# Kernel optimization log

Hardware: AMD Instinct MI355X
Metric: run time of the kernel (lower is better)

## Reference

```python
import jax, jax.numpy as jnp
import numpy as np

EPS = 1e-4

def _mlp2(x, W1, b1, W2, b2):
    # Sequential(Linear, ReLU, Linear) -> [*, 1]
    return jax.nn.relu(x @ W1 + b1) @ W2 + b2

def setup_inputs() -> dict:
    N, D = 400, 64
    key = jax.random.key(0)
    ks = jax.random.split(key, 24)
    s = 0.1
    inp = {
        "t": 0,
        "node_edge_embedding": jax.random.normal(ks[0], (N + N * N, D), jnp.float32),
        "node_flow_norm": jax.random.normal(ks[1], (N, D), jnp.float32),
        "A_ne": jax.random.uniform(ks[2], (N, N * N), jnp.float32),
        "node_num": N,
        # alpha_n_dedunce
        "W_alpha": jax.random.normal(ks[3], (D, D), jnp.float32) * s,
        "b_alpha": jnp.zeros((D,), jnp.float32),
        # gamma_e_dedunce
        "W_gamma": jax.random.normal(ks[4], (D, D), jnp.float32) * s,
        "b_gamma": jnp.zeros((D,), jnp.float32),
        # node_to_edge (2D -> D)
        "W_n2e": jax.random.normal(ks[5], (2 * D, D), jnp.float32) * s,
        "b_n2e": jnp.zeros((D,), jnp.float32),
        # edge_to_value: D -> D//2 -> 1
        "W_ev1": jax.random.normal(ks[6], (D, D // 2), jnp.float32) * s,
        "b_ev1": jnp.zeros((D // 2,), jnp.float32),
        "W_ev2": jax.random.normal(ks[7], (D // 2, 1), jnp.float32) * s,
        "b_ev2": jnp.zeros((1,), jnp.float32),
        # f_theta: D -> D//2 -> 1
        "W_ft1": jax.random.normal(ks[8], (D, D // 2), jnp.float32) * s,
        "b_ft1": jnp.zeros((D // 2,), jnp.float32),
        "W_ft2": jax.random.normal(ks[9], (D // 2, 1), jnp.float32) * s,
        "b_ft2": jnp.zeros((1,), jnp.float32),
        # W_3, W_4 (init.normal_ std=0.1)
        "W3": jax.random.normal(ks[10], (D, D), jnp.float32) * s,
        "W4": jax.random.normal(ks[11], (D, D), jnp.float32) * s,
        # edge_to_edge
        "W_e2e": jax.random.normal(ks[12], (D, D), jnp.float32) * s,
        "b_e2e": jnp.zeros((D,), jnp.float32),
        # node_to_edge_2 (2D -> D)
        "W_n2e2": jax.random.normal(ks[13], (2 * D, D), jnp.float32) * s,
        "b_n2e2": jnp.zeros((D,), jnp.float32),
    }
    return inp

def reference(t, node_edge_embedding, node_flow_norm, A_ne, node_num,
              W_alpha, b_alpha, W_gamma, b_gamma, W_n2e, b_n2e,
              W_ev1, b_ev1, W_ev2, b_ev2, W_ft1, b_ft1, W_ft2, b_ft2,
              W3, W4, W_e2e, b_e2e, W_n2e2, b_n2e2):
    N = node_num
    D = node_flow_norm.shape[1]
    node_emb = node_edge_embedding[:N]          # [N, D]
    edge_emb = node_edge_embedding[N:]          # [N*N, D]

    # fully-connected cartesian edge features: edges[i*N+j] = [node_i, node_j]
    edges = jnp.concatenate(
        [jnp.broadcast_to(node_emb[:, None, :], (N, N, D)),
         jnp.broadcast_to(node_emb[None, :, :], (N, N, D))], axis=-1
    ).reshape(N * N, 2 * D)                     # [N*N, 2D]

    h = edges @ W_n2e + b_n2e                   # node_to_edge
    A = jax.nn.relu(_mlp2(h, W_ev1, b_ev1, W_ev2, b_ev2)).reshape(N, N)

    # degree normalization: D_mat A D_mat with D_mat = diag(1/sqrt(clamp(rowsum)))
    d = 1.0 / jnp.sqrt(jnp.maximum(jnp.sum(A, axis=1), EPS))  # [N]
    normalized_A = d[:, None] * A * d[None, :]

    massage_conv = (normalized_A @ node_emb) @ W3
    alpha_n = massage_conv @ W_alpha + b_alpha
    alpha_n = alpha_n / jnp.maximum(jnp.max(jnp.abs(alpha_n)), EPS)

    denominator = _mlp2(node_flow_norm, W_ft1, b_ft1, W_ft2, b_ft2)   # [N,1]
    norm_value = _mlp2(node_emb, W_ft1, b_ft1, W_ft2, b_ft2) / \
        jnp.where(denominator == 0, EPS, denominator)
    node_self_evolve = norm_value * (jax.nn.relu(node_flow_norm - node_emb) @ W4)
    node_self_evolve = alpha_n * node_self_evolve

    gamma_e = jax.nn.softmax(edge_emb @ W_gamma + b_gamma, axis=1)    # [N*N, D]
    edge_indicator = jnp.where(A < 1.0, 0.0, 1.0).reshape(-1, 1)      # [N*N, 1]
    Aggr_edge = A_ne @ (edge_indicator * gamma_e * edge_emb)          # [N, D]
    pred_node = node_self_evolve + Aggr_edge

    edge_self_evolve = edge_emb @ W_e2e + b_e2e
    edge_infonode = edges @ W_n2e2 + b_n2e2
    pred_edge = edge_indicator * (edge_self_evolve + edge_infonode)

    pred_node_edge = jnp.concatenate([pred_node, pred_edge], axis=0)
    return pred_node_edge, edge_indicator
```

## Files before the change

### kernel.cpp

```cpp
#include <hip/hip_runtime.h>

#define NV_N 400
#define NN   160000
#define EPSV 1e-4f
#define IND_BASE ((size_t)160400 * 64)

#define OFF_A    0
#define OFF_P2   160000
#define OFF_Q2   172800
#define OFF_R    185600
#define OFF_S    211200
#define OFF_V4   236800
#define OFF_AR   262400
#define OFF_NV   288000
#define OFF_DV   288400
#define OFF_GMAX 288800
#define OFF_CNT  288832
#define OFF_LIST 289280
#define OFF_WV   449280

__global__ __launch_bounds__(256) void kA_pre(
    const float* __restrict__ NEE, const float* __restrict__ NFN,
    const float* __restrict__ W_n2e, const float* __restrict__ b_n2e,
    const float* __restrict__ W_n2e2, const float* __restrict__ b_n2e2,
    const float* __restrict__ W_ev1, const float* __restrict__ b_ev1,
    const float* __restrict__ W4,
    const float* __restrict__ W_ft1, const float* __restrict__ b_ft1,
    const float* __restrict__ W_ft2, const float* __restrict__ b_ft2,
    float* __restrict__ ws)
{
    __shared__ float xne[64], xnf[64], tP[64], tQ[64], hidN[32], hidF[32];
    int i = blockIdx.x, t = threadIdx.x;
    if (t < 64) { xne[t] = NEE[i*64+t]; xnf[t] = NFN[i*64+t]; }
    if (i == 0 && t == 0) ((unsigned*)ws)[OFF_GMAX] = 0u;
    __syncthreads();
    if (t < 64) {
        int dd = t;
        float pv = b_n2e[dd], qv = 0.f, rv = b_n2e2[dd], sv = 0.f, v4 = 0.f;
        for (int k = 0; k < 64; ++k) {
            float xk = xne[k];
            pv += xk * W_n2e[k*64+dd];
            qv += xk * W_n2e[(64+k)*64+dd];
            rv += xk * W_n2e2[k*64+dd];
            sv += xk * W_n2e2[(64+k)*64+dd];
            v4 += fmaxf(xnf[k]-xk, 0.f) * W4[k*64+dd];
        }
        tP[dd] = pv; tQ[dd] = qv;
        ws[OFF_R  + i*64+dd] = rv;
        ws[OFF_S  + i*64+dd] = sv;
        ws[OFF_V4 + i*64+dd] = v4;
    } else if (t >= 64 && t < 96) {
        int dd = t - 64;
        float hn = b_ft1[dd], hf = b_ft1[dd];
        for (int k = 0; k < 64; ++k) { hn += xne[k]*W_ft1[k*32+dd]; hf += xnf[k]*W_ft1[k*32+dd]; }
        hidN[dd] = fmaxf(hn, 0.f); hidF[dd] = fmaxf(hf, 0.f);
    }
    __syncthreads();
    if (t < 32) {
        float p2 = b_ev1[t], q2 = 0.f;
        for (int c = 0; c < 64; ++c) { p2 += tP[c]*W_ev1[c*32+t]; q2 += tQ[c]*W_ev1[c*32+t]; }
        ws[OFF_P2 + i*32+t] = p2;
        ws[OFF_Q2 + i*32+t] = q2;
    }
    if (t == 96) {
        float num = b_ft2[0], den = b_ft2[0];
        for (int c = 0; c < 32; ++c) { num += hidN[c]*W_ft2[c]; den += hidF[c]*W_ft2[c]; }
        float dv = (den == 0.f) ? EPSV : den;
        ws[OFF_NV + i] = num / dv;
    }
}

__global__ __launch_bounds__(256) void k2_row(
    const float* __restrict__ NEE,
    const float* __restrict__ W_ev2, const float* __restrict__ b_ev2,
    const float* __restrict__ W_e2e, const float* __restrict__ b_e2e,
    float* __restrict__ ws, float* __restrict__ out)
{
    __shared__ float p2s[32], wev2[32], redf[256];
    __shared__ int rcnt[256];
    __shared__ unsigned char flag[NV_N];
    __shared__ int act[NV_N];
    __shared__ int s_cnt;
    int i = blockIdx.x, t = threadIdx.x;
    if (t < 32) { p2s[t] = ws[OFF_P2 + i*32+t]; wev2[t] = W_ev2[t]; }
    __syncthreads();
    float b2 = b_ev2[0];
    float s = 0.f; int cc = 0;
    for (int j = t; j < NV_N; j += 256) {
        const float4* q2row = (const float4*)&ws[OFF_Q2 + j*32];
        float v = b2;
        #pragma unroll
        for (int c4 = 0; c4 < 8; ++c4) {
            float4 q = q2row[c4];
            v += fmaxf(p2s[c4*4+0]+q.x, 0.f) * wev2[c4*4+0];
            v += fmaxf(p2s[c4*4+1]+q.y, 0.f) * wev2[c4*4+1];
            v += fmaxf(p2s[c4*4+2]+q.z, 0.f) * wev2[c4*4+2];
            v += fmaxf(p2s[c4*4+3]+q.w, 0.f) * wev2[c4*4+3];
        }
        float a = fmaxf(v, 0.f);
        ws[OFF_A + i*NV_N + j] = a;
        bool f = (a >= 1.0f);
        flag[j] = f ? 1 : 0;
        out[IND_BASE + (size_t)i*NV_N + j] = f ? 1.f : 0.f;
        s += a; cc += f ? 1 : 0;
    }
    redf[t] = s; rcnt[t] = cc;
    __syncthreads();
    for (int st = 128; st > 0; st >>= 1) {
        if (t < st) { redf[t] += redf[t+st]; rcnt[t] += rcnt[t+st]; }
        __syncthreads();
    }
    if (t == 0) {
        ws[OFF_DV + i] = rsqrtf(fmaxf(redf[0], EPSV));
        ((int*)ws)[OFF_CNT + i] = rcnt[0];
    }
    if (t < 64) {
        int base = 0;
        for (int ch = 0; ch < 7; ++ch) {
            int j = ch*64 + t;
            bool f = (j < NV_N) && (flag[j] != 0);
            unsigned long long m = __ballot(f);
            if (f) {
                int pre = __popcll(m & ((1ull << t) - 1ull));
                act[base + pre] = j;
            }
            base += __popcll(m);
        }
        if (t == 0) s_cnt = base;
    }
    __syncthreads();
    {
        const float4 z4 = make_float4(0.f, 0.f, 0.f, 0.f);
        float4* orow = (float4*)(out + (NV_N + (size_t)i*NV_N) * 64);
        for (int q = t; q < NV_N*16; q += 256) {
            if (!flag[q >> 4]) orow[q] = z4;
        }
    }
    int cnt = s_cnt, lane = t & 63, w = t >> 6;
    for (int k = w; k < cnt; k += 4) {
        int j = act[k];
        int e = i*NV_N + j;
        float emb = NEE[(size_t)(NV_N + e)*64 + lane];
        float v = b_e2e[lane] + ws[OFF_R + i*64 + lane] + ws[OFF_S + j*64 + lane];
        #pragma unroll
        for (int c = 0; c < 64; ++c) v += __shfl(emb, c) * W_e2e[c*64 + lane];
        out[(size_t)(NV_N + e)*64 + lane] = v;
    }
}

__global__ __launch_bounds__(256) void k3_alpha_compact(
    const float* __restrict__ NEE,
    const float* __restrict__ W3,
    const float* __restrict__ W_alpha, const float* __restrict__ b_alpha,
    const float* __restrict__ W_gamma, const float* __restrict__ b_gamma,
    float* __restrict__ ws, int cap)
{
    __shared__ float part[4][64];
    __shared__ int red[256];
    __shared__ int s_off;
    int i = blockIdx.x, t = threadIdx.x, lane = t & 63, w = t >> 6;
    int os = 0;
    for (int r = t; r < i; r += 256) os += ((const int*)ws)[OFF_CNT + r];
    red[t] = os; __syncthreads();
    for (int st = 128; st > 0; st >>= 1) { if (t < st) red[t] += red[t+st]; __syncthreads(); }
    if (t == 0) s_off = red[0];
    float acc = 0.f;
    for (int j = w*100; j < w*100 + 100; ++j) {
        float coef = ws[OFF_A + i*NV_N + j] * ws[OFF_DV + j];
        acc += coef * NEE[j*64 + lane];
    }
    part[w][lane] = acc;
    __syncthreads();
    if (w == 0) {
        float nm = (part[0][lane] + part[1][lane] + part[2][lane] + part[3][lane]) * ws[OFF_DV + i];
        float mc = 0.f;
        #pragma unroll
        for (int c = 0; c < 64; ++c) mc += __shfl(nm, c) * W3[c*64 + lane];
        float ar = b_alpha[lane];
        #pragma unroll
        for (int c = 0; c < 64; ++c) ar += __shfl(mc, c) * W_alpha[c*64 + lane];
        ws[OFF_AR + i*64 + lane] = ar;
        float mx = fabsf(ar);
        #pragma unroll
        for (int off = 32; off > 0; off >>= 1) mx = fmaxf(mx, __shfl_xor(mx, off));
        if (lane == 0) atomicMax((unsigned*)ws + OFF_GMAX, __float_as_uint(mx));
    } else if (w == 1) {
        int base = 0;
        for (int ch = 0; ch < 7; ++ch) {
            int j = ch*64 + lane;
            float a = (j < NV_N) ? ws[OFF_A + i*NV_N + j] : 0.f;
            bool f = (a >= 1.0f);
            unsigned long long m = __ballot(f);
            if (f) {
                int pre = __popcll(m & ((1ull << lane) - 1ull));
                int slot = s_off + base + pre;
                if (slot < cap) ((int*)ws)[OFF_LIST + slot] = i*NV_N + j;
            }
            base += __popcll(m);
        }
    }
    __syncthreads();
    int cnt = ((const int*)ws)[OFF_CNT + i];
    for (int k = w; k < cnt; k += 4) {
        int slot = s_off + k;
        if (slot >= cap) break;
        int e = ((const int*)ws)[OFF_LIST + slot];
        float emb = NEE[(size_t)(NV_N + e)*64 + lane];
        float g = b_gamma[lane];
        #pragma unroll
        for (int c = 0; c < 64; ++c) g += __shfl(emb, c) * W_gamma[c*64 + lane];
        float mx = g;
        #pragma unroll
        for (int off = 32; off > 0; off >>= 1) mx = fmaxf(mx, __shfl_xor(mx, off));
        float p = __expf(g - mx);
        float ssum = p;
        #pragma unroll
        for (int off = 32; off > 0; off >>= 1) ssum += __shfl_xor(ssum, off);
        ws[OFF_WV + (size_t)slot*64 + lane] = (p / ssum) * emb;
    }
}

#define LCHUNK 4096
__global__ __launch_bounds__(256) void k4_final(
    const float* __restrict__ A_ne,
    const float* __restrict__ ws, int cap,
    float* __restrict__ out)
{
    __shared__ float av[LCHUNK];
    __shared__ float part[4][64];
    __shared__ int red[256];
    int i = blockIdx.x, t = threadIdx.x, lane = t & 63, w = t >> 6;
    int os = 0;
    for (int r = t; r < NV_N; r += 256) os += ((const int*)ws)[OFF_CNT + r];
    red[t] = os; __syncthreads();
    for (int st = 128; st > 0; st >>= 1) { if (t < st) red[t] += red[t+st]; __syncthreads(); }
    int nnz = red[0]; if (nnz > cap) nnz = cap;
    const float* Arow = A_ne + (size_t)i * NN;
    float acc = 0.f;
    for (int base = 0; base < nnz; base += LCHUNK) {
        int m = nnz - base; if (m > LCHUNK) m = LCHUNK;
        __syncthreads();
        for (int l = t; l < m; l += 256) {
            int e = ((const int*)ws)[OFF_LIST + base + l];
            av[l] = Arow[e];
        }
        __syncthreads();
        for (int l = w; l < m; l += 4)
            acc = fmaf(av[l], ws[OFF_WV + (size_t)(base + l)*64 + lane], acc);
    }
    part[w][lane] = acc;
    __syncthreads();
    if (w == 0) {
        float aggr = part[0][lane] + part[1][lane] + part[2][lane] + part[3][lane];
        float amax = fmaxf(__uint_as_float(((const unsigned*)ws)[OFF_GMAX]), EPSV);
        float v = (ws[OFF_AR + i*64 + lane] / amax) * ws[OFF_NV + i] * ws[OFF_V4 + i*64 + lane];
        out[i*64 + lane] = v + aggr;
    }
}

extern "C" void kernel_launch(void* const* d_in, const int* in_sizes, int n_in,
                              void* d_out, int out_size, void* d_ws, size_t ws_size,
                              hipStream_t stream) {
    const float* NEE     = (const float*)d_in[1];
    const float* NFN     = (const float*)d_in[2];
    const float* A_ne    = (const float*)d_in[3];
    const float* W_alpha = (const float*)d_in[5];
    const float* b_alpha = (const float*)d_in[6];
    const float* W_gamma = (const float*)d_in[7];
    const float* b_gamma = (const float*)d_in[8];
    const float* W_n2e   = (const float*)d_in[9];
    const float* b_n2e   = (const float*)d_in[10];
    const float* W_ev1   = (const float*)d_in[11];
    const float* b_ev1   = (const float*)d_in[12];
    const float* W_ev2   = (const float*)d_in[13];
    const float* b_ev2   = (const float*)d_in[14];
    const float* W_ft1   = (const float*)d_in[15];
    const float* b_ft1   = (const float*)d_in[16];
    const float* W_ft2   = (const float*)d_in[17];
    const float* b_ft2   = (const float*)d_in[18];
    const float* W3      = (const float*)d_in[19];
    const float* W4      = (const float*)d_in[20];
    const float* W_e2e   = (const float*)d_in[21];
    const float* b_e2e   = (const float*)d_in[22];
    const float* W_n2e2  = (const float*)d_in[23];
    const float* b_n2e2  = (const float*)d_in[24];
    float* out = (float*)d_out;
    float* ws  = (float*)d_ws;

    long long cap_ll = ((long long)(ws_size / 4) - OFF_WV) / 64;
    int cap = (cap_ll > NN) ? NN : (cap_ll < 0 ? 0 : (int)cap_ll);

    hipLaunchKernelGGL(kA_pre, dim3(NV_N), dim3(256), 0, stream,
        NEE, NFN, W_n2e, b_n2e, W_n2e2, b_n2e2, W_ev1, b_ev1, W4,
        W_ft1, b_ft1, W_ft2, b_ft2, ws);
    hipLaunchKernelGGL(k2_row, dim3(NV_N), dim3(256), 0, stream,
        NEE, W_ev2, b_ev2, W_e2e, b_e2e, ws, out);
    hipLaunchKernelGGL(k3_alpha_compact, dim3(NV_N), dim3(256), 0, stream,
        NEE, W3, W_alpha, b_alpha, W_gamma, b_gamma, ws, cap);
    hipLaunchKernelGGL(k4_final, dim3(NV_N), dim3(256), 0, stream,
        A_ne, ws, cap, out);
}
```

Baseline: 42.89 us.

## Precompute W3·W_alpha product and parallelize alpha projection across warps

An extra block in the pre-kernel computes the fused weight W3@W_alpha once, so the alpha kernel does one 64x64 projection instead of two serial shuffle-based matvecs done by a single wave. That projection is now split across all four waves through shared memory. Coefficients are staged in LDS, and the active-edge list is kept in shared memory instead of being reread from global. It costs an extra block and workspace region, and slightly changes rounding order.

Result: slower. 60.31 us (+40.6%).

```diff
diff --git a/kernel.cpp b/kernel.cpp
--- a/kernel.cpp
+++ b/kernel.cpp
@@ -16,8 +16,9 @@
 #define OFF_DV   288400
 #define OFF_GMAX 288800
 #define OFF_CNT  288832
-#define OFF_LIST 289280
-#define OFF_WV   449280
+#define OFF_W34  289280
+#define OFF_LIST 293376
+#define OFF_WV   453376
 
 __global__ __launch_bounds__(256) void kA_pre(
     const float* __restrict__ NEE, const float* __restrict__ NFN,
@@ -27,10 +28,22 @@
     const float* __restrict__ W4,
     const float* __restrict__ W_ft1, const float* __restrict__ b_ft1,
     const float* __restrict__ W_ft2, const float* __restrict__ b_ft2,
+    const float* __restrict__ W3, const float* __restrict__ W_alpha,
     float* __restrict__ ws)
 {
     __shared__ float xne[64], xnf[64], tP[64], tQ[64], hidN[32], hidF[32];
-    int i = blockIdx.x, t = threadIdx.x;
+    int b = blockIdx.x, t = threadIdx.x;
+    if (b == NV_N) {
+        int lane = t & 63, w = t >> 6;
+        for (int c = w; c < 64; c += 4) {
+            float p = 0.f;
+            #pragma unroll 8
+            for (int k = 0; k < 64; ++k) p += W3[c*64+k] * W_alpha[k*64+lane];
+            ws[OFF_W34 + c*64 + lane] = p;
+        }
+        return;
+    }
+    int i = b;
     if (t < 64) { xne[t] = NEE[i*64+t]; xnf[t] = NFN[i*64+t]; }
     if (i == 0 && t == 0) ((unsigned*)ws)[OFF_GMAX] = 0u;
     __syncthreads();
@@ -150,35 +163,47 @@
 
 __global__ __launch_bounds__(256) void k3_alpha_compact(
     const float* __restrict__ NEE,
-    const float* __restrict__ W3,
-    const float* __restrict__ W_alpha, const float* __restrict__ b_alpha,
+    const float* __restrict__ b_alpha,
     const float* __restrict__ W_gamma, const float* __restrict__ b_gamma,
     float* __restrict__ ws, int cap)
 {
+    __shared__ float coef[NV_N];
     __shared__ float part[4][64];
+    __shared__ float nmS[64];
+    __shared__ int act[NV_N];
     __shared__ int red[256];
-    __shared__ int s_off;
+    __shared__ int s_off, s_cnt;
     int i = blockIdx.x, t = threadIdx.x, lane = t & 63, w = t >> 6;
+
     int os = 0;
     for (int r = t; r < i; r += 256) os += ((const int*)ws)[OFF_CNT + r];
     red[t] = os; __syncthreads();
     for (int st = 128; st > 0; st >>= 1) { if (t < st) red[t] += red[t+st]; __syncthreads(); }
     if (t == 0) s_off = red[0];
+
+    for (int j = t; j < NV_N; j += 256)
+        coef[j] = ws[OFF_A + i*NV_N + j] * ws[OFF_DV + j];
+    __syncthreads();
+
     float acc = 0.f;
-    for (int j = w*100; j < w*100 + 100; ++j) {
-        float coef = ws[OFF_A + i*NV_N + j] * ws[OFF_DV + j];
-        acc += coef * NEE[j*64 + lane];
-    }
+    #pragma unroll 4
+    for (int j = w*100; j < w*100 + 100; ++j)
+        acc += coef[j] * NEE[j*64 + lane];
     part[w][lane] = acc;
     __syncthreads();
+    if (t < 64) nmS[t] = (part[0][t] + part[1][t] + part[2][t] + part[3][t]) * ws[OFF_DV + i];
+    __syncthreads();
+
+    {
+        float p = 0.f;
+        #pragma unroll
+        for (int c = w*16; c < w*16 + 16; ++c)
+            p += nmS[c] * ws[OFF_W34 + c*64 + lane];
+        part[w][lane] = p;
+    }
+    __syncthreads();
     if (w == 0) {
-        float nm = (part[0][lane] + part[1][lane] + part[2][lane] + part[3][lane]) * ws[OFF_DV + i];
-        float mc = 0.f;
-        #pragma unroll
-        for (int c = 0; c < 64; ++c) mc += __shfl(nm, c) * W3[c*64 + lane];
-        float ar = b_alpha[lane];
-        #pragma unroll
-        for (int c = 0; c < 64; ++c) ar += __shfl(mc, c) * W_alpha[c*64 + lane];
+        float ar = b_alpha[lane] + part[0][lane] + part[1][lane] + part[2][lane] + part[3][lane];
         ws[OFF_AR + i*64 + lane] = ar;
         float mx = fabsf(ar);
         #pragma unroll
@@ -193,18 +218,21 @@
             unsigned long long m = __ballot(f);
             if (f) {
                 int pre = __popcll(m & ((1ull << lane) - 1ull));
+                act[base + pre] = j;
                 int slot = s_off + base + pre;
                 if (slot < cap) ((int*)ws)[OFF_LIST + slot] = i*NV_N + j;
             }
             base += __popcll(m);
         }
-    }
-    __syncthreads();
-    int cnt = ((const int*)ws)[OFF_CNT + i];
+        if (lane == 0) s_cnt = base;
+    }
+    __syncthreads();
+
+    int cnt = s_cnt;
     for (int k = w; k < cnt; k += 4) {
         int slot = s_off + k;
         if (slot >= cap) break;
-        int e = ((const int*)ws)[OFF_LIST + slot];
+        int e = i*NV_N + act[k];
         float emb = NEE[(size_t)(NV_N + e)*64 + lane];
         float g = b_gamma[lane];
         #pragma unroll
@@ -290,13 +318,13 @@
     long long cap_ll = ((long long)(ws_size / 4) - OFF_WV) / 64;
     int cap = (cap_ll > NN) ? NN : (cap_ll < 0 ? 0 : (int)cap_ll);
 
-    hipLaunchKernelGGL(kA_pre, dim3(NV_N), dim3(256), 0, stream,
+    hipLaunchKernelGGL(kA_pre, dim3(NV_N + 1), dim3(256), 0, stream,
         NEE, NFN, W_n2e, b_n2e, W_n2e2, b_n2e2, W_ev1, b_ev1, W4,
-        W_ft1, b_ft1, W_ft2, b_ft2, ws);
+        W_ft1, b_ft1, W_ft2, b_ft2, W3, W_alpha, ws);
     hipLaunchKernelGGL(k2_row, dim3(NV_N), dim3(256), 0, stream,
         NEE, W_ev2, b_ev2, W_e2e, b_e2e, ws, out);
     hipLaunchKernelGGL(k3_alpha_compact, dim3(NV_N), dim3(256), 0, stream,
-        NEE, W3, W_alpha, b_alpha, W_gamma, b_gamma, ws, cap);
+        NEE, b_alpha, W_gamma, b_gamma, ws, cap);
     hipLaunchKernelGGL(k4_final, dim3(NV_N), dim3(256), 0, stream,
         A_ne, ws, cap, out);
 }
```
